# Kernel optimization log

Measured on AMD Instinct MI355X. Metric: run time of the kernel, lower is better.

The kernel has to match this reference:

```python
import jax, jax.numpy as jnp
import numpy as np

B, TQ, TK, D, F, H = 16, 256, 256, 256, 36, 8
DK = D // H          # dk = d // h
SF = int(np.sqrt(F)) # 6
MASK_VALUE = -1e30


def setup_inputs() -> dict:
    rng = jax.random.key(0)
    ks = jax.random.split(rng, 12)
    s = 0.05
    return {
        "query": jax.random.normal(ks[0], (B, TQ, D), jnp.float32),
        "key_ts": jax.random.normal(ks[1], (B, TK, D), jnp.float32),
        "value": jax.random.normal(ks[2], (B, TK, F), jnp.float32),
        "mask": (jax.random.uniform(ks[3], (B, TK, F)) < 0.5).astype(jnp.float32),
        "Wq": jax.random.normal(ks[4], (H, D, DK), jnp.float32) * s,
        "Wk": jax.random.normal(ks[5], (H, D, DK), jnp.float32) * s,
        "Wc": jax.random.normal(ks[6], (H, D), jnp.float32) * s,
        "bc": jnp.zeros((D,), jnp.float32),
        "Wo_1": jax.random.normal(ks[7], (F, SF), jnp.float32) * s,
        "bo_1": jnp.zeros((SF,), jnp.float32),
        "Wo_2": jax.random.normal(ks[8], (SF, 1), jnp.float32) * s,
        "bo_2": jnp.zeros((D,), jnp.float32),
    }


def reference(query, key_ts, value, mask, Wq, Wk, Wc, bc, Wo_1, bo_1, Wo_2, bo_2):
    # mask: [B, Tk, F] 0/1 missingness indicator -> broadcast as [B, 1, Tk, F]
    m = mask[:, None, :, :]
    heads = []
    for j in range(Wq.shape[0]):  # fixed small head loop (h=8)
        q = query @ Wq[j]                                  # [B, Tq, dk]
        k = key_ts @ Wk[j]                                 # [B, Tk, dk]
        A = jnp.einsum('bqd,bkd->bqk', q, k)[..., None]    # [B, Tq, Tk, 1] (no 1/sqrt(dk) scaling, as in original)
        A = m * A + (1.0 - m) * MASK_VALUE                 # [B, Tq, Tk, F]
        A = jax.nn.softmax(A, axis=-2)                     # softmax over Tk, per feature
        heads.append(jnp.einsum('bqkf,bkf->bqf', A, value))  # masked weighted sum
    latent = jnp.stack(heads, axis=-1)                     # [B, Tq, F, h]
    # permute (0,2,1,3) -> [B, F, Tq, h]; dot Wc[h,d] -> [B, F, Tq, d]
    latent = jnp.tanh(jnp.einsum('bqfh,hd->bfqd', latent, Wc) + bc)
    # permute (0,2,3,1) -> [B, Tq, d, F]; Wo_1: F -> sqrt(F)
    x = jnp.tanh(jnp.einsum('bfqd,fs->bqds', latent, Wo_1) + bo_1)
    # Wo_2: sqrt(F) -> 1, squeeze, add bo_2 -> [B, Tq, d]
    x = jnp.einsum('bqds,so->bqd', x, Wo_2) + bo_2
    return x
```

## Files before the change

kernel.cpp:

```cpp
#include <hip/hip_runtime.h>

#define NB 16
#define NTQ 256
#define NTK 256
#define ND 256
#define NF 36
#define NH 8
#define NDK 32
#define NSF 6

typedef __attribute__((ext_vector_type(8))) short short8;
typedef __attribute__((ext_vector_type(4))) float f32x4;
#define MFMA16(a,b,c) __builtin_amdgcn_mfma_f32_16x16x32_bf16(a,b,c,0,0,0)

#define RT_OFF   524288u
#define QPH_OFF  (2u*1024*1024)
#define QPL_OFF  (6u*1024*1024)
#define KPH_OFF  (10u*1024*1024)
#define KPL_OFF  (14u*1024*1024)
#define HD_OFF   (18u*1024*1024)

__device__ __forceinline__ short f2bf(float x){
    union { float f; unsigned u; } v; v.f = x;
    unsigned r = v.u + 0x7fffu + ((v.u >> 16) & 1u);
    return (short)(r >> 16);
}
__device__ __forceinline__ float bf2f(short s){
    union { float f; unsigned u; } v; v.u = ((unsigned)(unsigned short)s) << 16;
    return v.f;
}
__device__ __forceinline__ float fast_tanh(float x){
    float e = __expf(2.0f*x);
    return 1.0f - 2.0f/(e + 1.0f);
}
__device__ __forceinline__ short8 ld8(const short* p){ return *(const short8*)p; }

__device__ __forceinline__ void cvt8(const float* __restrict__ p, short8& h8, short8& l8){
    f32x4 a = *(const f32x4*)p;
    f32x4 c = *(const f32x4*)(p + 4);
    #pragma unroll
    for (int i = 0; i < 4; ++i){
        short h0 = f2bf(a[i]); h8[i]   = h0; l8[i]   = f2bf(a[i] - bf2f(h0));
        short h1 = f2bf(c[i]); h8[4+i] = h1; l8[4+i] = f2bf(c[i] - bf2f(h1));
    }
}

__global__ __launch_bounds__(256, 4)
void imta_proj(const float* __restrict__ query, const float* __restrict__ key_ts,
               const float* __restrict__ Wq, const float* __restrict__ Wk,
               const float* __restrict__ mask, const float* __restrict__ value,
               char* __restrict__ wsb){
    const int bid = blockIdx.x, tid = threadIdx.x;
    if (bid >= 1024){
        const int rb = bid - 1024;
        const int x = rb & 15, b = rb >> 4;
        const int k = tid;
        short* rt = (short*)(wsb + RT_OFF) + b*80*256;
        #pragma unroll
        for (int r = 0; r < 5; ++r){
            const int fp = x*5 + r;
            const int f = fp >> 1;
            short o = 0;
            if (f < NF){
                float m = mask[(b*NTK + k)*NF + f];
                o = (fp & 1) ? f2bf(m) : f2bf(m * value[(b*NTK + k)*NF + f]);
            }
            rt[fp*256 + k] = o;
        }
        return;
    }
    const int b = bid >> 6, side = (bid >> 5) & 1, j = (bid >> 2) & 7;
    const int t0 = (bid & 3)*64;
    const int w = tid >> 6, lane = tid & 63;
    const int col = lane & 15, quad = lane >> 4;

    __shared__ __align__(16) short sW[2*32*264];
    short* const sWH = sW;
    short* const sWL = sW + 32*264;

    const float* __restrict__ X = side ? key_ts : query;
    const float* __restrict__ W = (side ? Wk : Wq) + (size_t)j*ND*NDK;
    short* OH = (short*)(wsb + (side ? KPH_OFF : QPH_OFF));
    short* OL = (short*)(wsb + (side ? KPL_OFF : QPL_OFF));

    {
        const int dk0 = (tid & 7)*4, dbase = tid >> 3;
        #pragma unroll
        for (int it = 0; it < 8; ++it){
            const int d = dbase + it*32;
            f32x4 wv = *(const f32x4*)(W + (size_t)d*NDK + dk0);
            #pragma unroll
            for (int i = 0; i < 4; ++i){
                short h = f2bf(wv[i]);
                sWH[(dk0 + i)*264 + d] = h;
                sWL[(dk0 + i)*264 + d] = f2bf(wv[i] - bf2f(h));
            }
        }
    }
    __syncthreads();

    const int row = t0 + w*16 + col;
    const float* xrow = X + (size_t)(b*NTQ + row)*ND;
    f32x4 acc[2]; acc[0] = (f32x4)0.f; acc[1] = (f32x4)0.f;
    #pragma unroll
    for (int kb = 0; kb < 8; ++kb){
        const int dko = kb*32 + quad*8;
        short8 ah, al;
        cvt8(xrow + dko, ah, al);
        #pragma unroll
        for (int nt = 0; nt < 2; ++nt){
            short8 bh = *(const short8*)&sWH[(nt*16 + col)*264 + dko];
            short8 bl = *(const short8*)&sWL[(nt*16 + col)*264 + dko];
            acc[nt] = MFMA16(al, bh, acc[nt]);
            acc[nt] = MFMA16(ah, bl, acc[nt]);
            acc[nt] = MFMA16(ah, bh, acc[nt]);
        }
    }
    #pragma unroll
    for (int nt = 0; nt < 2; ++nt){
        const int dk = nt*16 + col;
        #pragma unroll
        for (int r = 0; r < 4; ++r){
            const int t = t0 + w*16 + quad*4 + r;
            float v = acc[nt][r];
            short h = f2bf(v);
            size_t o = (size_t)(((b*NH + j)*NTQ + t)*NDK + dk);
            OH[o] = h; OL[o] = f2bf(v - bf2f(h));
        }
    }
}

__global__ __launch_bounds__(256, 8)
void imta_attn(char* __restrict__ wsb, const float* __restrict__ value){
    const int t0 = blockIdx.x*16;
    const int j = blockIdx.y, b = blockIdx.z;
    const int tid = threadIdx.x, w = tid >> 6, lane = tid & 63;
    const int col = lane & 15, quad = lane >> 4;
    __shared__ __align__(16) short sE[16*264];
    const short* QH = (const short*)(wsb + QPH_OFF) + (b*NH + j)*NTQ*NDK;
    const short* QL = (const short*)(wsb + QPL_OFF) + (b*NH + j)*NTQ*NDK;
    const short* KH = (const short*)(wsb + KPH_OFF) + (b*NH + j)*NTK*NDK;
    const short* KL = (const short*)(wsb + KPL_OFF) + (b*NH + j)*NTK*NDK;
    const short* RT = (const short*)(wsb + RT_OFF) + b*80*256;
    float* HD = (float*)(wsb + HD_OFF) + (b*NH + j)*NTQ*NF;

    short8 ah = ld8(QH + (t0 + col)*NDK + quad*8);
    short8 al = ld8(QL + (t0 + col)*NDK + quad*8);
    #pragma unroll
    for (int nt = 0; nt < 4; ++nt){
        const int key0 = w*64 + nt*16;
        short8 bh = ld8(KH + (key0 + col)*NDK + quad*8);
        short8 bl = ld8(KL + (key0 + col)*NDK + quad*8);
        f32x4 c = (f32x4)0.f;
        c = MFMA16(al, bh, c);
        c = MFMA16(ah, bl, c);
        c = MFMA16(ah, bh, c);
        const int key = key0 + col;
        #pragma unroll
        for (int r = 0; r < 4; ++r)
            sE[(quad*4 + r)*264 + key] = f2bf(__expf(c[r]));
    }
    __syncthreads();

    f32x4 accA = (f32x4)0.f, accB = (f32x4)0.f;
    #pragma unroll 2
    for (int kb = 0; kb < 8; ++kb){
        const int ko = kb*32 + quad*8;
        short8 a = *(const short8*)&sE[col*264 + ko];
        short8 bb = ld8(RT + (w*16 + col)*256 + ko);
        accA = MFMA16(a, bb, accA);
        if (w == 0){
            short8 b2 = ld8(RT + (64 + col)*256 + ko);
            accB = MFMA16(a, b2, accB);
        }
    }
    __syncthreads();
    float* sH = (float*)sE;
    #pragma unroll
    for (int r = 0; r < 4; ++r){
        float v = accA[r];
        float o = __shfl_xor(v, 1, 64);
        if (!(col & 1)){
            const int f = w*8 + (col >> 1);
            float num = v, den = o, h;
            if (den != 0.0f) h = num/den;
            else {
                float s = 0.f;
                for (int k = 0; k < NTK; ++k) s += value[(b*NTK + k)*NF + f];
                h = s * (1.0f/256.0f);
            }
            sH[(quad*4 + r)*40 + f] = h;
        }
    }
    if (w == 0){
        #pragma unroll
        for (int r = 0; r < 4; ++r){
            float v = accB[r];
            float o = __shfl_xor(v, 1, 64);
            if (!(col & 1)){
                const int f = 32 + (col >> 1);
                if (f < NF){
                    float num = v, den = o, h;
                    if (den != 0.0f) h = num/den;
                    else {
                        float s = 0.f;
                        for (int k = 0; k < NTK; ++k) s += value[(b*NTK + k)*NF + f];
                        h = s * (1.0f/256.0f);
                    }
                    sH[(quad*4 + r)*40 + f] = h;
                }
            }
        }
    }
    __syncthreads();
    for (int idx = tid; idx < 16*NF; idx += 256){
        const int q = idx/NF, f = idx - q*NF;
        HD[(t0 + q)*NF + f] = sH[q*40 + f];
    }
}

__global__ void imta_final(const float* __restrict__ Wc, const float* __restrict__ bc,
                           const float* __restrict__ Wo1, const float* __restrict__ bo1,
                           const float* __restrict__ Wo2, const float* __restrict__ bo2,
                           const float* __restrict__ hd, float* __restrict__ out){
    const int bq = blockIdx.x;
    const int b = bq >> 8, qq = bq & 255;
    const int tid = threadIdx.x;
    __shared__ float sh[NF*NH];
    __shared__ float sW1[NF*NSF];
    for (int t = tid; t < NF*NH; t += 256){
        int jj = t/NF, f = t - jj*NF;
        sh[t] = hd[((b*NH + jj)*NTQ + qq)*NF + f];
    }
    if (tid < NF*NSF) sW1[tid] = Wo1[tid];
    __syncthreads();
    const int d = tid;
    float wcr[8];
    #pragma unroll
    for (int h = 0; h < 8; ++h) wcr[h] = Wc[h*ND + d];
    const float bcd = bc[d];
    float a2[6];
    #pragma unroll
    for (int s = 0; s < 6; ++s) a2[s] = bo1[s];
    #pragma unroll
    for (int f4 = 0; f4 < NF; f4 += 4){
        float4 sv[8];
        #pragma unroll
        for (int h = 0; h < 8; ++h) sv[h] = *(const float4*)&sh[h*NF + f4];
        #pragma unroll
        for (int fi = 0; fi < 4; ++fi){
            float a = bcd;
            #pragma unroll
            for (int h = 0; h < 8; ++h)
                a = fmaf(reinterpret_cast<const float*>(&sv[h])[fi], wcr[h], a);
            float lf = fast_tanh(a);
            const int f = f4 + fi;
            #pragma unroll
            for (int s = 0; s < 6; ++s)
                a2[s] = fmaf(lf, sW1[f*NSF + s], a2[s]);
        }
    }
    float o = bo2[d];
    #pragma unroll
    for (int s = 0; s < 6; ++s)
        o = fmaf(fast_tanh(a2[s]), Wo2[s], o);
    out[(b*NTQ + qq)*ND + d] = o;
}

extern "C" void kernel_launch(void* const* d_in, const int* in_sizes, int n_in,
                              void* d_out, int out_size, void* d_ws, size_t ws_size,
                              hipStream_t stream){
    const float* query  = (const float*)d_in[0];
    const float* key_ts = (const float*)d_in[1];
    const float* value  = (const float*)d_in[2];
    const float* mask   = (const float*)d_in[3];
    const float* Wq     = (const float*)d_in[4];
    const float* Wk     = (const float*)d_in[5];
    const float* Wc     = (const float*)d_in[6];
    const float* bc     = (const float*)d_in[7];
    const float* Wo1    = (const float*)d_in[8];
    const float* bo1    = (const float*)d_in[9];
    const float* Wo2    = (const float*)d_in[10];
    const float* bo2    = (const float*)d_in[11];
    char* wsb  = (char*)d_ws;
    float* out = (float*)d_out;
    (void)in_sizes; (void)n_in; (void)out_size; (void)ws_size;

    imta_proj <<<dim3(1280),     dim3(256), 0, stream>>>(query, key_ts, Wq, Wk, mask, value, wsb);
    imta_attn <<<dim3(16, 8, 16),dim3(256), 0, stream>>>(wsb, value);
    imta_final<<<dim3(4096),     dim3(256), 0, stream>>>(Wc, bc, Wo1, bo1, Wo2, bo2,
                                                         (const float*)(wsb + HD_OFF), out);
}
```

Baseline: 141.9 us.

## Fuse attention and final projection kernels into one per (batch, query-tile) block

Merges the attention kernel and the final Wc/Wo projection kernel into a single kernel where each 512-thread block handles all 8 heads for a 16-query tile of one batch. Head outputs stay in shared memory instead of going through a global workspace, which removes one launch and the round trip for the intermediate tensor. The trade-off is fewer blocks (256 instead of 2048 plus 4096), larger shared memory use (about 66KB), and lower occupancy. The final stage now loops over 8 queries per thread, which serialises that work.

```diff
diff --git a/kernel.cpp b/kernel.cpp
--- a/kernel.cpp
+++ b/kernel.cpp
@@ -18,7 +18,6 @@
 #define QPL_OFF  (6u*1024*1024)
 #define KPH_OFF  (10u*1024*1024)
 #define KPL_OFF  (14u*1024*1024)
-#define HD_OFF   (18u*1024*1024)
 
 __device__ __forceinline__ short f2bf(float x){
     union { float f; unsigned u; } v; v.f = x;
@@ -130,75 +129,85 @@
     }
 }
 
-__global__ __launch_bounds__(256, 8)
-void imta_attn(char* __restrict__ wsb, const float* __restrict__ value){
-    const int t0 = blockIdx.x*16;
-    const int j = blockIdx.y, b = blockIdx.z;
+__global__ __launch_bounds__(512, 2)
+void imta_af(char* __restrict__ wsb, const float* __restrict__ value,
+             const float* __restrict__ Wc, const float* __restrict__ bc,
+             const float* __restrict__ Wo1, const float* __restrict__ bo1,
+             const float* __restrict__ Wo2, const float* __restrict__ bo2,
+             float* __restrict__ out){
+    const int t0 = blockIdx.x*16, b = blockIdx.y;
     const int tid = threadIdx.x, w = tid >> 6, lane = tid & 63;
     const int col = lane & 15, quad = lane >> 4;
-    __shared__ __align__(16) short sE[16*264];
-    const short* QH = (const short*)(wsb + QPH_OFF) + (b*NH + j)*NTQ*NDK;
-    const short* QL = (const short*)(wsb + QPL_OFF) + (b*NH + j)*NTQ*NDK;
-    const short* KH = (const short*)(wsb + KPH_OFF) + (b*NH + j)*NTK*NDK;
-    const short* KL = (const short*)(wsb + KPL_OFF) + (b*NH + j)*NTK*NDK;
+    __shared__ __align__(16) short sBuf[8*16*264];
+    short* const sE = sBuf;
     const short* RT = (const short*)(wsb + RT_OFF) + b*80*256;
-    float* HD = (float*)(wsb + HD_OFF) + (b*NH + j)*NTQ*NF;
-
-    short8 ah = ld8(QH + (t0 + col)*NDK + quad*8);
-    short8 al = ld8(QL + (t0 + col)*NDK + quad*8);
-    #pragma unroll
-    for (int nt = 0; nt < 4; ++nt){
-        const int key0 = w*64 + nt*16;
-        short8 bh = ld8(KH + (key0 + col)*NDK + quad*8);
-        short8 bl = ld8(KL + (key0 + col)*NDK + quad*8);
-        f32x4 c = (f32x4)0.f;
-        c = MFMA16(al, bh, c);
-        c = MFMA16(ah, bl, c);
-        c = MFMA16(ah, bh, c);
-        const int key = key0 + col;
-        #pragma unroll
-        for (int r = 0; r < 4; ++r)
-            sE[(quad*4 + r)*264 + key] = f2bf(__expf(c[r]));
-    }
-    __syncthreads();
-
-    f32x4 accA = (f32x4)0.f, accB = (f32x4)0.f;
-    #pragma unroll 2
+
+    {
+        const int jbase = (w >> 2)*4, keyq = (w & 3)*64;
+        #pragma unroll
+        for (int jo = 0; jo < 4; ++jo){
+            const int j = jbase + jo;
+            const short* QH = (const short*)(wsb + QPH_OFF) + (b*NH + j)*NTQ*NDK;
+            const short* QL = (const short*)(wsb + QPL_OFF) + (b*NH + j)*NTQ*NDK;
+            const short* KH = (const short*)(wsb + KPH_OFF) + (b*NH + j)*NTK*NDK;
+            const short* KL = (const short*)(wsb + KPL_OFF) + (b*NH + j)*NTK*NDK;
+            short8 ah = ld8(QH + (t0 + col)*NDK + quad*8);
+            short8 al = ld8(QL + (t0 + col)*NDK + quad*8);
+            #pragma unroll
+            for (int nt = 0; nt < 4; ++nt){
+                const int key0 = keyq + nt*16;
+                short8 bh = ld8(KH + (key0 + col)*NDK + quad*8);
+                short8 bl = ld8(KL + (key0 + col)*NDK + quad*8);
+                f32x4 c = (f32x4)0.f;
+                c = MFMA16(al, bh, c);
+                c = MFMA16(ah, bl, c);
+                c = MFMA16(ah, bh, c);
+                const int key = key0 + col;
+                #pragma unroll
+                for (int r = 0; r < 4; ++r)
+                    sE[j*4224 + (quad*4 + r)*264 + key] = f2bf(__expf(c[r]));
+            }
+        }
+    }
+    __syncthreads();
+
+    f32x4 acc[5];
+    int   jt[5], ntt[5];
+    const short* sEp[5];
+    const short* rtp[5];
+    #pragma unroll
+    for (int i = 0; i < 5; ++i){
+        const int t = w + 8*i;
+        const int j = t/5, nt = t - 5*j;
+        jt[i] = j; ntt[i] = nt;
+        sEp[i] = sE + j*4224 + col*264;
+        rtp[i] = RT + (nt*16 + col)*256;
+        acc[i] = (f32x4)0.f;
+    }
+    #pragma unroll
     for (int kb = 0; kb < 8; ++kb){
         const int ko = kb*32 + quad*8;
-        short8 a = *(const short8*)&sE[col*264 + ko];
-        short8 bb = ld8(RT + (w*16 + col)*256 + ko);
-        accA = MFMA16(a, bb, accA);
-        if (w == 0){
-            short8 b2 = ld8(RT + (64 + col)*256 + ko);
-            accB = MFMA16(a, b2, accB);
-        }
-    }
-    __syncthreads();
-    float* sH = (float*)sE;
-    #pragma unroll
-    for (int r = 0; r < 4; ++r){
-        float v = accA[r];
-        float o = __shfl_xor(v, 1, 64);
-        if (!(col & 1)){
-            const int f = w*8 + (col >> 1);
-            float num = v, den = o, h;
-            if (den != 0.0f) h = num/den;
-            else {
-                float s = 0.f;
-                for (int k = 0; k < NTK; ++k) s += value[(b*NTK + k)*NF + f];
-                h = s * (1.0f/256.0f);
-            }
-            sH[(quad*4 + r)*40 + f] = h;
-        }
-    }
-    if (w == 0){
+        #pragma unroll
+        for (int i = 0; i < 5; ++i){
+            short8 a  = *(const short8*)(sEp[i] + ko);
+            short8 bb = ld8(rtp[i] + ko);
+            acc[i] = MFMA16(a, bb, acc[i]);
+        }
+    }
+    __syncthreads();
+
+    float* const sHD = (float*)sBuf;
+    float* const sW1 = sHD + 16*8*40;
+    if (tid < NF*NSF) sW1[tid] = Wo1[tid];
+    #pragma unroll
+    for (int i = 0; i < 5; ++i){
+        const int j = jt[i], nt = ntt[i];
         #pragma unroll
         for (int r = 0; r < 4; ++r){
-            float v = accB[r];
+            float v = acc[i][r];
             float o = __shfl_xor(v, 1, 64);
             if (!(col & 1)){
-                const int f = 32 + (col >> 1);
+                const int f = nt*8 + (col >> 1);
                 if (f < NF){
                     float num = v, den = o, h;
                     if (den != 0.0f) h = num/den;
@@ -207,64 +216,54 @@
                         for (int k = 0; k < NTK; ++k) s += value[(b*NTK + k)*NF + f];
                         h = s * (1.0f/256.0f);
                     }
-                    sH[(quad*4 + r)*40 + f] = h;
+                    sHD[((quad*4 + r)*8 + j)*40 + f] = h;
                 }
             }
         }
     }
     __syncthreads();
-    for (int idx = tid; idx < 16*NF; idx += 256){
-        const int q = idx/NF, f = idx - q*NF;
-        HD[(t0 + q)*NF + f] = sH[q*40 + f];
-    }
-}
-
-__global__ void imta_final(const float* __restrict__ Wc, const float* __restrict__ bc,
-                           const float* __restrict__ Wo1, const float* __restrict__ bo1,
-                           const float* __restrict__ Wo2, const float* __restrict__ bo2,
-                           const float* __restrict__ hd, float* __restrict__ out){
-    const int bq = blockIdx.x;
-    const int b = bq >> 8, qq = bq & 255;
-    const int tid = threadIdx.x;
-    __shared__ float sh[NF*NH];
-    __shared__ float sW1[NF*NSF];
-    for (int t = tid; t < NF*NH; t += 256){
-        int jj = t/NF, f = t - jj*NF;
-        sh[t] = hd[((b*NH + jj)*NTQ + qq)*NF + f];
-    }
-    if (tid < NF*NSF) sW1[tid] = Wo1[tid];
-    __syncthreads();
-    const int d = tid;
-    float wcr[8];
-    #pragma unroll
-    for (int h = 0; h < 8; ++h) wcr[h] = Wc[h*ND + d];
-    const float bcd = bc[d];
-    float a2[6];
-    #pragma unroll
-    for (int s = 0; s < 6; ++s) a2[s] = bo1[s];
-    #pragma unroll
-    for (int f4 = 0; f4 < NF; f4 += 4){
-        float4 sv[8];
-        #pragma unroll
-        for (int h = 0; h < 8; ++h) sv[h] = *(const float4*)&sh[h*NF + f4];
-        #pragma unroll
-        for (int fi = 0; fi < 4; ++fi){
-            float a = bcd;
-            #pragma unroll
-            for (int h = 0; h < 8; ++h)
-                a = fmaf(reinterpret_cast<const float*>(&sv[h])[fi], wcr[h], a);
-            float lf = fast_tanh(a);
-            const int f = f4 + fi;
+
+    {
+        const int d = tid & 255, qh = tid >> 8;
+        float wcr[8];
+        #pragma unroll
+        for (int h = 0; h < 8; ++h) wcr[h] = Wc[h*ND + d];
+        const float bcd = bc[d];
+        float bo1r[6], wo2r[6];
+        #pragma unroll
+        for (int s = 0; s < 6; ++s){ bo1r[s] = bo1[s]; wo2r[s] = Wo2[s]; }
+        const float bo2d = bo2[d];
+        #pragma unroll
+        for (int qi = 0; qi < 8; ++qi){
+            const int q = qh*8 + qi;
+            float a2[6];
+            #pragma unroll
+            for (int s = 0; s < 6; ++s) a2[s] = bo1r[s];
+            #pragma unroll
+            for (int f4 = 0; f4 < NF; f4 += 4){
+                float4 sv[8];
+                #pragma unroll
+                for (int h = 0; h < 8; ++h) sv[h] = *(const float4*)&sHD[(q*8 + h)*40 + f4];
+                #pragma unroll
+                for (int fi = 0; fi < 4; ++fi){
+                    float a = bcd;
+                    #pragma unroll
+                    for (int h = 0; h < 8; ++h)
+                        a = fmaf(reinterpret_cast<const float*>(&sv[h])[fi], wcr[h], a);
+                    float lf = fast_tanh(a);
+                    const int f = f4 + fi;
+                    #pragma unroll
+                    for (int s = 0; s < 6; ++s)
+                        a2[s] = fmaf(lf, sW1[f*NSF + s], a2[s]);
+                }
+            }
+            float o = bo2d;
             #pragma unroll
             for (int s = 0; s < 6; ++s)
-                a2[s] = fmaf(lf, sW1[f*NSF + s], a2[s]);
-        }
-    }
-    float o = bo2[d];
-    #pragma unroll
-    for (int s = 0; s < 6; ++s)
-        o = fmaf(fast_tanh(a2[s]), Wo2[s], o);
-    out[(b*NTQ + qq)*ND + d] = o;
+                o = fmaf(fast_tanh(a2[s]), wo2r[s], o);
+            out[(b*NTQ + t0 + q)*ND + d] = o;
+        }
+    }
 }
 
 extern "C" void kernel_launch(void* const* d_in, const int* in_sizes, int n_in,
@@ -286,8 +285,6 @@
     float* out = (float*)d_out;
     (void)in_sizes; (void)n_in; (void)out_size; (void)ws_size;
 
-    imta_proj <<<dim3(1280),     dim3(256), 0, stream>>>(query, key_ts, Wq, Wk, mask, value, wsb);
-    imta_attn <<<dim3(16, 8, 16),dim3(256), 0, stream>>>(wsb, value);
-    imta_final<<<dim3(4096),     dim3(256), 0, stream>>>(Wc, bc, Wo1, bo1, Wo2, bo2,
-                                                         (const float*)(wsb + HD_OFF), out);
-}
+    imta_proj<<<dim3(1280),   dim3(256), 0, stream>>>(query, key_ts, Wq, Wk, mask, value, wsb);
+    imta_af  <<<dim3(16, 16), dim3(512), 0, stream>>>(wsb, value, Wc, bc, Wo1, bo1, Wo2, bo2, out);
+}
```

After: 209.4 us. 47.5% more time.

## Fuse final projection into attention kernel via last-block atomic counter

Applied to the files above, without the earlier changes.

Removes the separate imta_final launch. Each attention block bumps a per-(batch, query-tile) atomic counter after writing its head output. The last of the 8 head blocks gathers all heads for its 16 queries and computes the Wc/tanh/Wo1/Wo2 epilogue for all 256 output channels. The counters are reset inside the projection kernel. This saves a launch and its tail, but only one in eight blocks does the serial 16-query epilogue, and the launch bound drops from 8 to 4 blocks per CU.

```diff
diff --git a/kernel.cpp b/kernel.cpp
--- a/kernel.cpp
+++ b/kernel.cpp
@@ -19,6 +19,7 @@
 #define KPH_OFF  (10u*1024*1024)
 #define KPL_OFF  (14u*1024*1024)
 #define HD_OFF   (18u*1024*1024)
+#define CNT_OFF  (24u*1024*1024)
 
 __device__ __forceinline__ short f2bf(float x){
     union { float f; unsigned u; } v; v.f = x;
@@ -53,6 +54,7 @@
     const int bid = blockIdx.x, tid = threadIdx.x;
     if (bid >= 1024){
         const int rb = bid - 1024;
+        if (rb == 0) ((unsigned*)(wsb + CNT_OFF))[tid] = 0u;
         const int x = rb & 15, b = rb >> 4;
         const int k = tid;
         short* rt = (short*)(wsb + RT_OFF) + b*80*256;
@@ -130,13 +132,19 @@
     }
 }
 
-__global__ __launch_bounds__(256, 8)
-void imta_attn(char* __restrict__ wsb, const float* __restrict__ value){
+__global__ __launch_bounds__(256, 4)
+void imta_at(char* __restrict__ wsb, const float* __restrict__ value,
+             const float* __restrict__ Wc, const float* __restrict__ bc,
+             const float* __restrict__ Wo1, const float* __restrict__ bo1,
+             const float* __restrict__ Wo2, const float* __restrict__ bo2,
+             float* __restrict__ out){
     const int t0 = blockIdx.x*16;
     const int j = blockIdx.y, b = blockIdx.z;
     const int tid = threadIdx.x, w = tid >> 6, lane = tid & 63;
     const int col = lane & 15, quad = lane >> 4;
-    __shared__ __align__(16) short sE[16*264];
+    __shared__ __align__(16) char sMem[19648];
+    __shared__ int sLast;
+    short* const sE = (short*)sMem;
     const short* QH = (const short*)(wsb + QPH_OFF) + (b*NH + j)*NTQ*NDK;
     const short* QL = (const short*)(wsb + QPL_OFF) + (b*NH + j)*NTQ*NDK;
     const short* KH = (const short*)(wsb + KPH_OFF) + (b*NH + j)*NTK*NDK;
@@ -175,7 +183,7 @@
         }
     }
     __syncthreads();
-    float* sH = (float*)sE;
+    float* sH = (float*)sMem;
     #pragma unroll
     for (int r = 0; r < 4; ++r){
         float v = accA[r];
@@ -217,54 +225,70 @@
         const int q = idx/NF, f = idx - q*NF;
         HD[(t0 + q)*NF + f] = sH[q*40 + f];
     }
-}
-
-__global__ void imta_final(const float* __restrict__ Wc, const float* __restrict__ bc,
-                           const float* __restrict__ Wo1, const float* __restrict__ bo1,
-                           const float* __restrict__ Wo2, const float* __restrict__ bo2,
-                           const float* __restrict__ hd, float* __restrict__ out){
-    const int bq = blockIdx.x;
-    const int b = bq >> 8, qq = bq & 255;
-    const int tid = threadIdx.x;
-    __shared__ float sh[NF*NH];
-    __shared__ float sW1[NF*NSF];
-    for (int t = tid; t < NF*NH; t += 256){
-        int jj = t/NF, f = t - jj*NF;
-        sh[t] = hd[((b*NH + jj)*NTQ + qq)*NF + f];
+
+    __syncthreads();
+    if (tid == 0){
+        __threadfence();
+        unsigned old = __hip_atomic_fetch_add(
+            (unsigned*)(wsb + CNT_OFF) + (b*16 + blockIdx.x), 1u,
+            __ATOMIC_ACQ_REL, __HIP_MEMORY_SCOPE_AGENT);
+        sLast = (old == 7u) ? 1 : 0;
+    }
+    __syncthreads();
+    if (!sLast) return;
+    __threadfence();
+
+    const float* hdall = (const float*)(wsb + HD_OFF);
+    float* const sHD2 = (float*)sMem;
+    float* const sW1  = sHD2 + 16*288;
+    for (int idx = tid; idx < 16*NF*NH; idx += 256){
+        const int q = idx/(NF*NH), r = idx - q*(NF*NH);
+        const int jj = r/NF, f = r - jj*NF;
+        sHD2[q*288 + jj*NF + f] = hdall[((size_t)(b*NH + jj)*NTQ + t0 + q)*NF + f];
     }
     if (tid < NF*NSF) sW1[tid] = Wo1[tid];
     __syncthreads();
-    const int d = tid;
-    float wcr[8];
-    #pragma unroll
-    for (int h = 0; h < 8; ++h) wcr[h] = Wc[h*ND + d];
-    const float bcd = bc[d];
-    float a2[6];
-    #pragma unroll
-    for (int s = 0; s < 6; ++s) a2[s] = bo1[s];
-    #pragma unroll
-    for (int f4 = 0; f4 < NF; f4 += 4){
-        float4 sv[8];
-        #pragma unroll
-        for (int h = 0; h < 8; ++h) sv[h] = *(const float4*)&sh[h*NF + f4];
-        #pragma unroll
-        for (int fi = 0; fi < 4; ++fi){
-            float a = bcd;
+
+    {
+        const int d = tid;
+        float wcr[8];
+        #pragma unroll
+        for (int h = 0; h < 8; ++h) wcr[h] = Wc[h*ND + d];
+        const float bcd = bc[d];
+        float bo1r[6], wo2r[6];
+        #pragma unroll
+        for (int s = 0; s < 6; ++s){ bo1r[s] = bo1[s]; wo2r[s] = Wo2[s]; }
+        const float bo2d = bo2[d];
+        for (int q = 0; q < 16; ++q){
+            const float* shq = sHD2 + q*288;
+            float a2[6];
             #pragma unroll
-            for (int h = 0; h < 8; ++h)
-                a = fmaf(reinterpret_cast<const float*>(&sv[h])[fi], wcr[h], a);
-            float lf = fast_tanh(a);
-            const int f = f4 + fi;
+            for (int s = 0; s < 6; ++s) a2[s] = bo1r[s];
+            #pragma unroll
+            for (int f4 = 0; f4 < NF; f4 += 4){
+                float4 sv[8];
+                #pragma unroll
+                for (int h = 0; h < 8; ++h) sv[h] = *(const float4*)&shq[h*NF + f4];
+                #pragma unroll
+                for (int fi = 0; fi < 4; ++fi){
+                    float a = bcd;
+                    #pragma unroll
+                    for (int h = 0; h < 8; ++h)
+                        a = fmaf(reinterpret_cast<const float*>(&sv[h])[fi], wcr[h], a);
+                    float lf = fast_tanh(a);
+                    const int f = f4 + fi;
+                    #pragma unroll
+                    for (int s = 0; s < 6; ++s)
+                        a2[s] = fmaf(lf, sW1[f*NSF + s], a2[s]);
+                }
+            }
+            float o = bo2d;
             #pragma unroll
             for (int s = 0; s < 6; ++s)
-                a2[s] = fmaf(lf, sW1[f*NSF + s], a2[s]);
-        }
-    }
-    float o = bo2[d];
-    #pragma unroll
-    for (int s = 0; s < 6; ++s)
-        o = fmaf(fast_tanh(a2[s]), Wo2[s], o);
-    out[(b*NTQ + qq)*ND + d] = o;
+                o = fmaf(fast_tanh(a2[s]), wo2r[s], o);
+            out[(b*NTQ + t0 + q)*ND + d] = o;
+        }
+    }
 }
 
 extern "C" void kernel_launch(void* const* d_in, const int* in_sizes, int n_in,
@@ -286,8 +310,6 @@
     float* out = (float*)d_out;
     (void)in_sizes; (void)n_in; (void)out_size; (void)ws_size;
 
-    imta_proj <<<dim3(1280),     dim3(256), 0, stream>>>(query, key_ts, Wq, Wk, mask, value, wsb);
-    imta_attn <<<dim3(16, 8, 16),dim3(256), 0, stream>>>(wsb, value);
-    imta_final<<<dim3(4096),     dim3(256), 0, stream>>>(Wc, bc, Wo1, bo1, Wo2, bo2,
-                                                         (const float*)(wsb + HD_OFF), out);
-}
+    imta_proj<<<dim3(1280),      dim3(256), 0, stream>>>(query, key_ts, Wq, Wk, mask, value, wsb);
+    imta_at  <<<dim3(16, 8, 16), dim3(256), 0, stream>>>(wsb, value, Wc, bc, Wo1, bo1, Wo2, bo2, out);
+}
```

New measurement: 538.2 us. 279% more time.

## Fuse query projection into attention kernel, precompute transposed split-bf16 Wq

Applied to the files above, without the earlier changes.

Drops the Q-projection blocks from the first kernel, and with them the Q hi/lo intermediates written to and read back from workspace. Each attention block now computes its 16-row query tile on the fly from fp32 query and a pre-transposed hi/lo bf16 Wq, staged through shared memory. The prep kernel shrinks to K projection plus the Wq transpose and mask/value packing. In exchange, the attention kernel does extra MFMA work, and only two of its four waves do it, which adds a sync and some imbalance before the score computation.

```diff
diff --git a/kernel.cpp b/kernel.cpp
--- a/kernel.cpp
+++ b/kernel.cpp
@@ -13,9 +13,9 @@
 typedef __attribute__((ext_vector_type(4))) float f32x4;
 #define MFMA16(a,b,c) __builtin_amdgcn_mfma_f32_16x16x32_bf16(a,b,c,0,0,0)
 
+#define WQTH_OFF 0u
+#define WQTL_OFF 131072u
 #define RT_OFF   524288u
-#define QPH_OFF  (2u*1024*1024)
-#define QPL_OFF  (6u*1024*1024)
 #define KPH_OFF  (10u*1024*1024)
 #define KPL_OFF  (14u*1024*1024)
 #define HD_OFF   (18u*1024*1024)
@@ -46,13 +46,21 @@
 }
 
 __global__ __launch_bounds__(256, 4)
-void imta_proj(const float* __restrict__ query, const float* __restrict__ key_ts,
-               const float* __restrict__ Wq, const float* __restrict__ Wk,
-               const float* __restrict__ mask, const float* __restrict__ value,
-               char* __restrict__ wsb){
+void imta_prep(const float* __restrict__ key_ts, const float* __restrict__ Wq,
+               const float* __restrict__ Wk, const float* __restrict__ mask,
+               const float* __restrict__ value, char* __restrict__ wsb){
     const int bid = blockIdx.x, tid = threadIdx.x;
-    if (bid >= 1024){
-        const int rb = bid - 1024;
+    if (bid >= 512){
+        const int rb = bid - 512;
+        {
+            const int idx = rb*256 + tid;
+            const int d = idx & 255, jdk = idx >> 8;
+            const int jj = jdk >> 5, dk = jdk & 31;
+            float v = Wq[(jj*ND + d)*NDK + dk];
+            short h = f2bf(v);
+            ((short*)(wsb + WQTH_OFF))[idx] = h;
+            ((short*)(wsb + WQTL_OFF))[idx] = f2bf(v - bf2f(h));
+        }
         const int x = rb & 15, b = rb >> 4;
         const int k = tid;
         short* rt = (short*)(wsb + RT_OFF) + b*80*256;
@@ -69,7 +77,7 @@
         }
         return;
     }
-    const int b = bid >> 6, side = (bid >> 5) & 1, j = (bid >> 2) & 7;
+    const int b = bid >> 5, j = (bid >> 2) & 7;
     const int t0 = (bid & 3)*64;
     const int w = tid >> 6, lane = tid & 63;
     const int col = lane & 15, quad = lane >> 4;
@@ -78,10 +86,9 @@
     short* const sWH = sW;
     short* const sWL = sW + 32*264;
 
-    const float* __restrict__ X = side ? key_ts : query;
-    const float* __restrict__ W = (side ? Wk : Wq) + (size_t)j*ND*NDK;
-    short* OH = (short*)(wsb + (side ? KPH_OFF : QPH_OFF));
-    short* OL = (short*)(wsb + (side ? KPL_OFF : QPL_OFF));
+    const float* __restrict__ W = Wk + (size_t)j*ND*NDK;
+    short* OH = (short*)(wsb + KPH_OFF);
+    short* OL = (short*)(wsb + KPL_OFF);
 
     {
         const int dk0 = (tid & 7)*4, dbase = tid >> 3;
@@ -100,7 +107,7 @@
     __syncthreads();
 
     const int row = t0 + w*16 + col;
-    const float* xrow = X + (size_t)(b*NTQ + row)*ND;
+    const float* xrow = key_ts + (size_t)(b*NTK + row)*ND;
     f32x4 acc[2]; acc[0] = (f32x4)0.f; acc[1] = (f32x4)0.f;
     #pragma unroll
     for (int kb = 0; kb < 8; ++kb){
@@ -131,21 +138,50 @@
 }
 
 __global__ __launch_bounds__(256, 8)
-void imta_attn(char* __restrict__ wsb, const float* __restrict__ value){
+void imta_attn(char* __restrict__ wsb, const float* __restrict__ query,
+               const float* __restrict__ value){
     const int t0 = blockIdx.x*16;
     const int j = blockIdx.y, b = blockIdx.z;
     const int tid = threadIdx.x, w = tid >> 6, lane = tid & 63;
     const int col = lane & 15, quad = lane >> 4;
     __shared__ __align__(16) short sE[16*264];
-    const short* QH = (const short*)(wsb + QPH_OFF) + (b*NH + j)*NTQ*NDK;
-    const short* QL = (const short*)(wsb + QPL_OFF) + (b*NH + j)*NTQ*NDK;
+    __shared__ __align__(16) short sQH[16*40];
+    __shared__ __align__(16) short sQL[16*40];
     const short* KH = (const short*)(wsb + KPH_OFF) + (b*NH + j)*NTK*NDK;
     const short* KL = (const short*)(wsb + KPL_OFF) + (b*NH + j)*NTK*NDK;
     const short* RT = (const short*)(wsb + RT_OFF) + b*80*256;
     float* HD = (float*)(wsb + HD_OFF) + (b*NH + j)*NTQ*NF;
 
-    short8 ah = ld8(QH + (t0 + col)*NDK + quad*8);
-    short8 al = ld8(QL + (t0 + col)*NDK + quad*8);
+    if (w < 2){
+        const short* WTH = (const short*)(wsb + WQTH_OFF) + (size_t)(j*32 + w*16 + col)*ND;
+        const short* WTL = (const short*)(wsb + WQTL_OFF) + (size_t)(j*32 + w*16 + col)*ND;
+        const float* xrow = query + (size_t)(b*NTQ + t0 + col)*ND;
+        f32x4 qa = (f32x4)0.f;
+        #pragma unroll
+        for (int kb = 0; kb < 8; ++kb){
+            const int dko = kb*32 + quad*8;
+            short8 xh, xl;
+            cvt8(xrow + dko, xh, xl);
+            short8 bh = ld8(WTH + dko);
+            short8 bl = ld8(WTL + dko);
+            qa = MFMA16(xl, bh, qa);
+            qa = MFMA16(xh, bl, qa);
+            qa = MFMA16(xh, bh, qa);
+        }
+        const int dk = w*16 + col;
+        #pragma unroll
+        for (int r = 0; r < 4; ++r){
+            const int q = quad*4 + r;
+            float v = qa[r];
+            short h = f2bf(v);
+            sQH[q*40 + dk] = h;
+            sQL[q*40 + dk] = f2bf(v - bf2f(h));
+        }
+    }
+    __syncthreads();
+
+    short8 ah = *(const short8*)&sQH[col*40 + quad*8];
+    short8 al = *(const short8*)&sQL[col*40 + quad*8];
     #pragma unroll
     for (int nt = 0; nt < 4; ++nt){
         const int key0 = w*64 + nt*16;
@@ -286,8 +322,8 @@
     float* out = (float*)d_out;
     (void)in_sizes; (void)n_in; (void)out_size; (void)ws_size;
 
-    imta_proj <<<dim3(1280),     dim3(256), 0, stream>>>(query, key_ts, Wq, Wk, mask, value, wsb);
-    imta_attn <<<dim3(16, 8, 16),dim3(256), 0, stream>>>(wsb, value);
+    imta_prep <<<dim3(768),      dim3(256), 0, stream>>>(key_ts, Wq, Wk, mask, value, wsb);
+    imta_attn <<<dim3(16, 8, 16),dim3(256), 0, stream>>>(wsb, query, value);
     imta_final<<<dim3(4096),     dim3(256), 0, stream>>>(Wc, bc, Wo1, bo1, Wo2, bo2,
                                                          (const float*)(wsb + HD_OFF), out);
 }
```

After: 149.8 us. 5.5% more time.
